# Kernel optimization log

Hardware: AMD Instinct MI355X
Metric: run time of the kernel (lower is better)

## Reference

```python
import jax, jax.numpy as jnp
import numpy as np

TEXT_DIM = 4096
FEATURE_DIM = 4096


def _xavier_uniform(key, shape):
    fan_in, fan_out = shape[1], shape[0]
    limit = float(np.sqrt(6.0 / (fan_in + fan_out)))
    return jax.random.uniform(key, shape, jnp.float32, -limit, limit)


def setup_inputs() -> dict:
    key = jax.random.key(0)
    k1, k2, k3, k4 = jax.random.split(key, 4)
    text = jax.random.normal(k1, (8, 2048, TEXT_DIM), jnp.float32)
    features = jax.random.normal(k2, (8, 576, FEATURE_DIM), jnp.float32)
    # nn.Linear weights: [out, in]; biases initialized to 0
    Wq = _xavier_uniform(k3, (FEATURE_DIM, TEXT_DIM))
    bq = jnp.zeros((FEATURE_DIM,), jnp.float32)
    Wk = _xavier_uniform(k4, (FEATURE_DIM, FEATURE_DIM))
    bk = jnp.zeros((FEATURE_DIM,), jnp.float32)
    return {"text": text, "features": features, "Wq": Wq, "bq": bq, "Wk": Wk, "bk": bk}


def reference(text, features, Wq, bq, Wk, bk):
    # Q: [b, t, d], K: [b, p, d]
    Q = jnp.einsum('btx,dx->btd', text, Wq) + bq
    K = jnp.einsum('bpx,dx->bpd', features, Wk) + bk
    scale = 1.0 / jnp.sqrt(jnp.asarray(K.shape[-1], K.dtype))
    scores = jnp.einsum('btd,bpd->btp', Q, K) * scale  # [b, t, p]
    attn = jax.nn.softmax(scores, axis=-1)
    attended = jnp.einsum('btp,bpd->btd', attn, features)  # [b, t, d]
    return attended
```

## Files before the change

kernel.cpp:

```cpp
#include <hip/hip_runtime.h>
#include <hip/hip_bf16.h>
#include <stdint.h>

#define DEVI __device__ __forceinline__

typedef __attribute__((ext_vector_type(8))) __bf16 bf16x8;
typedef __attribute__((ext_vector_type(4))) float f32x4;

DEVI unsigned short f2b(float f) {
  union { float f; unsigned int u; } x; x.f = f;
  unsigned int u = x.u;
  return (unsigned short)((u + 0x7fffu + ((u >> 16) & 1u)) >> 16);
}

__global__ void cvt_kernel(const float* __restrict__ in,
                           unsigned short* __restrict__ out, long n4) {
  long i = (long)blockIdx.x * blockDim.x + threadIdx.x;
  long stride = (long)gridDim.x * blockDim.x;
  for (; i < n4; i += stride) {
    float4 v = reinterpret_cast<const float4*>(in)[i];
    ushort4 o;
    o.x = f2b(v.x); o.y = f2b(v.y); o.z = f2b(v.z); o.w = f2b(v.w);
    reinterpret_cast<ushort4*>(out)[i] = o;
  }
}

__global__ void transpose_cvt_kernel(const float* __restrict__ in,
                                     unsigned short* __restrict__ out,
                                     int P, int D) {
  __shared__ unsigned short tile[32][33];
  int b = blockIdx.z;
  int d0 = blockIdx.x * 32, p0 = blockIdx.y * 32;
  const float* src = in + (long)b * P * D;
  unsigned short* dst = out + (long)b * D * P;
  int tx = threadIdx.x & 31, ty = threadIdx.x >> 5;
  for (int i = 0; i < 32; i += 8)
    tile[ty + i][tx] = f2b(src[(long)(p0 + ty + i) * D + d0 + tx]);
  __syncthreads();
  for (int i = 0; i < 32; i += 8)
    dst[(long)(d0 + ty + i) * P + p0 + tx] = tile[tx][ty + i];
}

__global__ void gemv_col_kernel(const float* __restrict__ W,
                                const float* __restrict__ v,
                                float* __restrict__ u, int D) {
  int y = blockIdx.x * 256 + threadIdx.x;
  int d0 = blockIdx.y * 128;
  float s = 0.f;
  for (int d = d0; d < d0 + 128; ++d) s += W[(long)d * D + y] * v[d];
  atomicAdd(&u[y], s);
}

__global__ void rowdot_kernel(const float* __restrict__ feat,
                              const float* __restrict__ u,
                              float* __restrict__ c, int D) {
  long row = (long)blockIdx.x * 4 + (threadIdx.x >> 6);
  int lane = threadIdx.x & 63;
  const float4* fr = (const float4*)(feat + row * D);
  const float4* uv = (const float4*)u;
  float s = 0.f;
  for (int j = lane; j < D / 4; j += 64) {
    float4 f = fr[j], g = uv[j];
    s += f.x * g.x + f.y * g.y + f.z * g.z + f.w * g.w;
  }
#pragma unroll
  for (int o = 32; o > 0; o >>= 1) s += __shfl_xor(s, o, 64);
  if (lane == 0) c[row] = s;
}

DEVI void gll16(const void* g, void* l) {
  __builtin_amdgcn_global_load_lds(
      (const __attribute__((address_space(1))) unsigned int*)g,
      (__attribute__((address_space(3))) unsigned int*)l, 16, 0, 0);
}

template<int OUT_BF16, int HAS_BIAS, int BATCH_X,
         int WM, int WN, int ACCM, int ACCN, int WAVES_EU>
__global__ __launch_bounds__(256, WAVES_EU) void gemm_nt_kernel(
    const unsigned short* __restrict__ A,
    const unsigned short* __restrict__ B,
    void* __restrict__ Cv,
    const float* __restrict__ bias,
    float scale, int M, int N, int K,
    long sA, long sB, long sC, long sBias) {
  constexpr int NW = WM * WN;
  constexpr int SA = WM * ACCM;
  constexpr int SB = WN * ACCN;
  constexpr int CA2 = SA * 2 / NW;
  constexpr int CB2 = SB * 2 / NW;
  static_assert(CA2 * NW == SA * 2 && CB2 * NW == SB * 2, "issue divisibility");

  __shared__ unsigned short As[SA * 1024];
  __shared__ unsigned short Bs[SB * 1024];

  const int tid = threadIdx.x;
  const int lane = tid & 63;
  const int wid = tid >> 6;
  const int wm = wid / WN;
  const int wn = wid % WN;

  int bx = blockIdx.x;
  int b;
  if (BATCH_X) { b = bx & 7; bx >>= 3; } else { b = blockIdx.z; }
  const int n0 = bx * (SB * 16);
  const int m0 = blockIdx.y * (SA * 16);

  const unsigned short* Ab = A + (long)b * sA;
  const unsigned short* Bb = B + (long)b * sB;
  const float* biasb = HAS_BIAS ? bias + (long)b * sBias : nullptr;

  const int r8 = lane >> 3;
  const int csw = ((lane & 7) ^ r8) * 8;

  auto stage = [&](int k0) {
#pragma unroll
    for (int t = 0; t < CA2; ++t) {
      const int a = wid * CA2 + t, j = a >> 1, i = a & 1;
      gll16(Ab + (long)(m0 + j * 16 + i * 8 + r8) * K + k0 + csw,
            (void*)(As + j * 1024 + i * 512));
    }
#pragma unroll
    for (int t = 0; t < CB2; ++t) {
      const int a = wid * CB2 + t, j = a >> 1, i = a & 1;
      gll16(Bb + (long)(n0 + j * 16 + i * 8 + r8) * K + k0 + csw,
            (void*)(Bs + j * 1024 + i * 512));
    }
  };

  f32x4 acc[ACCM][ACCN];
#pragma unroll
  for (int m = 0; m < ACCM; ++m)
#pragma unroll
    for (int n = 0; n < ACCN; ++n) acc[m][n] = (f32x4){0.f, 0.f, 0.f, 0.f};

  const int lrow = lane & 15;
  const int x7 = lane & 7;
  const int g = lane >> 4;
  const int so0 = ((g) ^ x7) * 8;
  const int so1 = ((4 + g) ^ x7) * 8;
  const int wmA = wm * ACCM * 16;
  const int wnB = wn * ACCN * 16;

  for (int k0 = 0; k0 < K; k0 += 64) {
    stage(k0);
    __syncthreads();

#pragma unroll
    for (int s = 0; s < 2; ++s) {
      const int so = s ? so1 : so0;
      bf16x8 af[ACCM], bfr[ACCN];
#pragma unroll
      for (int m = 0; m < ACCM; ++m)
        af[m] = *reinterpret_cast<const bf16x8*>(
            &As[(wmA + m * 16 + lrow) * 64 + so]);
#pragma unroll
      for (int n = 0; n < ACCN; ++n)
        bfr[n] = *reinterpret_cast<const bf16x8*>(
            &Bs[(wnB + n * 16 + lrow) * 64 + so]);
#pragma unroll
      for (int m = 0; m < ACCM; ++m)
#pragma unroll
        for (int n = 0; n < ACCN; ++n)
          acc[m][n] = __builtin_amdgcn_mfma_f32_16x16x32_bf16(af[m], bfr[n], acc[m][n], 0, 0, 0);
    }

    __syncthreads();
  }

  const int crow = (lane >> 4) * 4;
  const int ccol = lane & 15;
#pragma unroll
  for (int m = 0; m < ACCM; ++m) {
#pragma unroll
    for (int n = 0; n < ACCN; ++n) {
      const int gc = n0 + wn * ACCN * 16 + n * 16 + ccol;
      float bv = HAS_BIAS ? biasb[gc] : 0.f;
#pragma unroll
      for (int r = 0; r < 4; ++r) {
        const int gr = m0 + wm * ACCM * 16 + m * 16 + crow + r;
        float v = (acc[m][n][r] + bv) * scale;
        long off = (long)b * sC + (long)gr * N + gc;
        if (OUT_BF16)
          ((unsigned short*)Cv)[off] = f2b(v);
        else
          ((float*)Cv)[off] = v;
      }
    }
  }
}

__global__ void softmax_kernel(const float* __restrict__ s,
                               unsigned short* __restrict__ attn) {
  const int P = 576;
  long row = (long)blockIdx.x * 4 + (threadIdx.x >> 6);
  int lane = threadIdx.x & 63;
  const float* sr = s + row * P;
  unsigned short* ar = attn + row * P;
  float v[9];
  float mx = -3.0e38f;
#pragma unroll
  for (int j = 0; j < 9; ++j) {
    v[j] = sr[j * 64 + lane];
    mx = fmaxf(mx, v[j]);
  }
#pragma unroll
  for (int o = 32; o > 0; o >>= 1) mx = fmaxf(mx, __shfl_xor(mx, o, 64));
  float sum = 0.f;
#pragma unroll
  for (int j = 0; j < 9; ++j) {
    v[j] = __expf(v[j] - mx);
    sum += v[j];
  }
#pragma unroll
  for (int o = 32; o > 0; o >>= 1) sum += __shfl_xor(sum, o, 64);
  float inv = 1.0f / sum;
#pragma unroll
  for (int j = 0; j < 9; ++j) ar[j * 64 + lane] = f2b(v[j] * inv);
}

extern "C" void kernel_launch(void* const* d_in, const int* in_sizes, int n_in,
                              void* d_out, int out_size, void* d_ws, size_t ws_size,
                              hipStream_t stream) {
  const float* text = (const float*)d_in[0];
  const float* feat = (const float*)d_in[1];
  const float* Wq = (const float*)d_in[2];
  const float* bq = (const float*)d_in[3];
  const float* Wk = (const float*)d_in[4];
  const float* bk = (const float*)d_in[5];
  (void)bk;

  const int B = 8, T = 2048, P = 576, D = 4096;
  const long nText = (long)B * T * D;
  const long nFeat = (long)B * P * D;

  char* ws = (char*)d_ws;
  unsigned short* text_b = (unsigned short*)(ws);
  unsigned short* feat_b = (unsigned short*)(ws + 134217728);
  unsigned short* fT_b   = (unsigned short*)(ws + 171966464);
  unsigned short* WqT_b  = (unsigned short*)(ws + 209715200);
  unsigned short* WkT_b  = (unsigned short*)(ws + 243269632);
  unsigned short* attn_b = (unsigned short*)(ws + 276824064);
  float* u               = (float*)(ws + 295698432);
  float* c               = (float*)(ws + 295714816);
  float* scores          = (float*)(ws + 209715200);
  unsigned short* W2T_b  = (unsigned short*)d_out;
  unsigned short* KW_b   = (unsigned short*)((char*)d_out + 67108864);

  dim3 blk(256);
  cvt_kernel<<<4096, blk, 0, stream>>>(text, text_b, nText / 4);
  cvt_kernel<<<2048, blk, 0, stream>>>(feat, feat_b, nFeat / 4);
  transpose_cvt_kernel<<<dim3(D / 32, P / 32, B), blk, 0, stream>>>(feat, fT_b, P, D);
  transpose_cvt_kernel<<<dim3(D / 32, D / 32, 1), blk, 0, stream>>>(Wq, WqT_b, D, D);
  transpose_cvt_kernel<<<dim3(D / 32, D / 32, 1), blk, 0, stream>>>(Wk, WkT_b, D, D);
  hipMemsetAsync(u, 0, D * sizeof(float), stream);
  gemv_col_kernel<<<dim3(D / 256, 32), blk, 0, stream>>>(Wk, bq, u, D);
  rowdot_kernel<<<(B * P) / 4, blk, 0, stream>>>(feat, u, c, D);

  gemm_nt_kernel<1, 0, 0, 2, 2, 4, 4, 4><<<dim3(32, 32, 1), blk, 0, stream>>>(
      WqT_b, WkT_b, W2T_b, nullptr, 1.0f, D, D, D, 0, 0, 0, 0);
  gemm_nt_kernel<1, 0, 0, 2, 2, 4, 4, 4><<<dim3(32, 36, 1), blk, 0, stream>>>(
      feat_b, W2T_b, KW_b, nullptr, 1.0f, B * P, D, D, 0, 0, 0, 0);
  gemm_nt_kernel<0, 1, 1, 2, 2, 8, 2, 4><<<dim3(72, 8), blk, 0, stream>>>(
      text_b, KW_b, scores, c, 1.0f / 64.0f, T, P, D,
      (long)T * D, (long)P * D, (long)T * P, P);
  softmax_kernel<<<(B * T) / 4, blk, 0, stream>>>(scores, attn_b);
  gemm_nt_kernel<0, 0, 1, 2, 2, 4, 4, 4><<<dim3(256, 16), blk, 0, stream>>>(
      attn_b, fT_b, (float*)d_out, nullptr, 1.0f, T, D, P,
      (long)T * P, (long)D * P, (long)T * D, 0);
}
```

Before: 759.2 us.

## Double-buffer LDS in weight GEMMs and fuse feature convert with transpose

Adds an optional double-buffered LDS pipeline to the GEMM kernel, so the next K tile is fetched with global_load_lds while the current tile runs through MFMA. It is enabled only for the two large weight-product GEMMs, whose occupancy hint drops from 4 to 2 waves per EU to make room for the doubled shared memory. The features array is now converted to bf16 in normal and transposed layouts by one kernel, so the fp32 source is read once instead of twice. The risks are lower occupancy and a narrower write pattern for the non-transposed output than the old vectorized converter used.

```diff
diff --git a/kernel.cpp b/kernel.cpp
--- a/kernel.cpp
+++ b/kernel.cpp
@@ -41,6 +41,27 @@
     dst[(long)(d0 + ty + i) * P + p0 + tx] = tile[tx][ty + i];
 }
 
+__global__ void feat_cvt_tr_kernel(const float* __restrict__ in,
+                                   unsigned short* __restrict__ outN,
+                                   unsigned short* __restrict__ outT,
+                                   int P, int D) {
+  __shared__ unsigned short tile[32][33];
+  int b = blockIdx.z;
+  int d0 = blockIdx.x * 32, p0 = blockIdx.y * 32;
+  const float* src = in + (long)b * P * D;
+  unsigned short* dstN = outN + (long)b * P * D;
+  unsigned short* dstT = outT + (long)b * D * P;
+  int tx = threadIdx.x & 31, ty = threadIdx.x >> 5;
+  for (int i = 0; i < 32; i += 8) {
+    unsigned short v = f2b(src[(long)(p0 + ty + i) * D + d0 + tx]);
+    tile[ty + i][tx] = v;
+    dstN[(long)(p0 + ty + i) * D + d0 + tx] = v;
+  }
+  __syncthreads();
+  for (int i = 0; i < 32; i += 8)
+    dstT[(long)(d0 + ty + i) * P + p0 + tx] = tile[tx][ty + i];
+}
+
 __global__ void gemv_col_kernel(const float* __restrict__ W,
                                 const float* __restrict__ v,
                                 float* __restrict__ u, int D) {
@@ -75,7 +96,7 @@
 }
 
 template<int OUT_BF16, int HAS_BIAS, int BATCH_X,
-         int WM, int WN, int ACCM, int ACCN, int WAVES_EU>
+         int WM, int WN, int ACCM, int ACCN, int WAVES_EU, int DBUF>
 __global__ __launch_bounds__(256, WAVES_EU) void gemm_nt_kernel(
     const unsigned short* __restrict__ A,
     const unsigned short* __restrict__ B,
@@ -88,10 +109,11 @@
   constexpr int SB = WN * ACCN;
   constexpr int CA2 = SA * 2 / NW;
   constexpr int CB2 = SB * 2 / NW;
+  constexpr int NB = DBUF ? 2 : 1;
   static_assert(CA2 * NW == SA * 2 && CB2 * NW == SB * 2, "issue divisibility");
 
-  __shared__ unsigned short As[SA * 1024];
-  __shared__ unsigned short Bs[SB * 1024];
+  __shared__ unsigned short As[NB][SA * 1024];
+  __shared__ unsigned short Bs[NB][SB * 1024];
 
   const int tid = threadIdx.x;
   const int lane = tid & 63;
@@ -112,18 +134,18 @@
   const int r8 = lane >> 3;
   const int csw = ((lane & 7) ^ r8) * 8;
 
-  auto stage = [&](int k0) {
+  auto stage = [&](int k0, int buf) {
 #pragma unroll
     for (int t = 0; t < CA2; ++t) {
       const int a = wid * CA2 + t, j = a >> 1, i = a & 1;
       gll16(Ab + (long)(m0 + j * 16 + i * 8 + r8) * K + k0 + csw,
-            (void*)(As + j * 1024 + i * 512));
+            (void*)(As[buf] + j * 1024 + i * 512));
     }
 #pragma unroll
     for (int t = 0; t < CB2; ++t) {
       const int a = wid * CB2 + t, j = a >> 1, i = a & 1;
       gll16(Bb + (long)(n0 + j * 16 + i * 8 + r8) * K + k0 + csw,
-            (void*)(Bs + j * 1024 + i * 512));
+            (void*)(Bs[buf] + j * 1024 + i * 512));
     }
   };
 
@@ -141,10 +163,7 @@
   const int wmA = wm * ACCM * 16;
   const int wnB = wn * ACCN * 16;
 
-  for (int k0 = 0; k0 < K; k0 += 64) {
-    stage(k0);
-    __syncthreads();
-
+  auto compute = [&](int buf) {
 #pragma unroll
     for (int s = 0; s < 2; ++s) {
       const int so = s ? so1 : so0;
@@ -152,19 +171,36 @@
 #pragma unroll
       for (int m = 0; m < ACCM; ++m)
         af[m] = *reinterpret_cast<const bf16x8*>(
-            &As[(wmA + m * 16 + lrow) * 64 + so]);
+            &As[buf][(wmA + m * 16 + lrow) * 64 + so]);
 #pragma unroll
       for (int n = 0; n < ACCN; ++n)
         bfr[n] = *reinterpret_cast<const bf16x8*>(
-            &Bs[(wnB + n * 16 + lrow) * 64 + so]);
+            &Bs[buf][(wnB + n * 16 + lrow) * 64 + so]);
 #pragma unroll
       for (int m = 0; m < ACCM; ++m)
 #pragma unroll
         for (int n = 0; n < ACCN; ++n)
           acc[m][n] = __builtin_amdgcn_mfma_f32_16x16x32_bf16(af[m], bfr[n], acc[m][n], 0, 0, 0);
     }
-
+  };
+
+  if (DBUF) {
+    stage(0, 0);
     __syncthreads();
+    int cur = 0;
+    for (int k0 = 0; k0 < K; k0 += 64) {
+      if (k0 + 64 < K) stage(k0 + 64, cur ^ 1);
+      compute(cur);
+      __syncthreads();
+      cur ^= 1;
+    }
+  } else {
+    for (int k0 = 0; k0 < K; k0 += 64) {
+      stage(k0, 0);
+      __syncthreads();
+      compute(0);
+      __syncthreads();
+    }
   }
 
   const int crow = (lane >> 4) * 4;
@@ -248,23 +284,22 @@
 
   dim3 blk(256);
   cvt_kernel<<<4096, blk, 0, stream>>>(text, text_b, nText / 4);
-  cvt_kernel<<<2048, blk, 0, stream>>>(feat, feat_b, nFeat / 4);
-  transpose_cvt_kernel<<<dim3(D / 32, P / 32, B), blk, 0, stream>>>(feat, fT_b, P, D);
+  feat_cvt_tr_kernel<<<dim3(D / 32, P / 32, B), blk, 0, stream>>>(feat, feat_b, fT_b, P, D);
   transpose_cvt_kernel<<<dim3(D / 32, D / 32, 1), blk, 0, stream>>>(Wq, WqT_b, D, D);
   transpose_cvt_kernel<<<dim3(D / 32, D / 32, 1), blk, 0, stream>>>(Wk, WkT_b, D, D);
   hipMemsetAsync(u, 0, D * sizeof(float), stream);
   gemv_col_kernel<<<dim3(D / 256, 32), blk, 0, stream>>>(Wk, bq, u, D);
   rowdot_kernel<<<(B * P) / 4, blk, 0, stream>>>(feat, u, c, D);
 
-  gemm_nt_kernel<1, 0, 0, 2, 2, 4, 4, 4><<<dim3(32, 32, 1), blk, 0, stream>>>(
+  gemm_nt_kernel<1, 0, 0, 2, 2, 4, 4, 2, 1><<<dim3(32, 32, 1), blk, 0, stream>>>(
       WqT_b, WkT_b, W2T_b, nullptr, 1.0f, D, D, D, 0, 0, 0, 0);
-  gemm_nt_kernel<1, 0, 0, 2, 2, 4, 4, 4><<<dim3(32, 36, 1), blk, 0, stream>>>(
+  gemm_nt_kernel<1, 0, 0, 2, 2, 4, 4, 2, 1><<<dim3(32, 36, 1), blk, 0, stream>>>(
       feat_b, W2T_b, KW_b, nullptr, 1.0f, B * P, D, D, 0, 0, 0, 0);
-  gemm_nt_kernel<0, 1, 1, 2, 2, 8, 2, 4><<<dim3(72, 8), blk, 0, stream>>>(
+  gemm_nt_kernel<0, 1, 1, 2, 2, 8, 2, 4, 0><<<dim3(72, 8), blk, 0, stream>>>(
       text_b, KW_b, scores, c, 1.0f / 64.0f, T, P, D,
       (long)T * D, (long)P * D, (long)T * P, P);
   softmax_kernel<<<(B * T) / 4, blk, 0, stream>>>(scores, attn_b);
-  gemm_nt_kernel<0, 0, 1, 2, 2, 4, 4, 4><<<dim3(256, 16), blk, 0, stream>>>(
+  gemm_nt_kernel<0, 0, 1, 2, 2, 4, 4, 4, 0><<<dim3(256, 16), blk, 0, stream>>>(
       attn_b, fT_b, (float*)d_out, nullptr, 1.0f, T, D, P,
       (long)T * P, (long)D * P, (long)T * D, 0);
 }
```

Result: slower. 849.4 us (+11.9%).
